# Kernel optimization log

Measured on AMD Instinct MI355X. Metric: run time of the kernel, lower is better.

## Reference

```python
import math
import jax, jax.numpy as jnp
import numpy as np

N_HEADS = 8
FACTOR = 1


def setup_inputs() -> dict:
    key = jax.random.key(0)
    ks = jax.random.split(key, 8)
    B, L, D = 8, 2048, 512
    scale = 0.05
    return {
        "queries": jax.random.normal(ks[0], (B, L, D), jnp.float32),
        "keys": jax.random.normal(ks[1], (B, L, D), jnp.float32),
        "values": jax.random.normal(ks[2], (B, L, D), jnp.float32),
        "Wq": jax.random.normal(ks[3], (D, D), jnp.float32) * scale,
        "bq": jnp.zeros((D,), jnp.float32),
        "Wk": jax.random.normal(ks[4], (D, D), jnp.float32) * scale,
        "bk": jnp.zeros((D,), jnp.float32),
        "Wv": jax.random.normal(ks[5], (D, D), jnp.float32) * scale,
        "bv": jnp.zeros((D,), jnp.float32),
        "Wo": jax.random.normal(ks[6], (D, D), jnp.float32) * scale,
        "bo": jnp.zeros((D,), jnp.float32),
    }


def _autocorrelation(q, k, v):
    # q,k,v: [B, L, H, E]; L == S assumed (as built in setup_inputs)
    B, L, H, E = q.shape
    qp = jnp.transpose(q, (0, 2, 3, 1))  # [B,H,E,L]
    kp = jnp.transpose(k, (0, 2, 3, 1))
    vp = jnp.transpose(v, (0, 2, 3, 1))
    q_fft = jnp.fft.rfft(qp, axis=-1)
    k_fft = jnp.fft.rfft(kp, axis=-1)
    corr = jnp.fft.irfft(q_fft * jnp.conj(k_fft), n=L, axis=-1)  # [B,H,E,L]

    # training-path time-delay aggregation
    top_k = int(FACTOR * math.log(L))  # static python int
    mean_value = corr.mean(axis=(1, 2))  # [B, L]
    _, index = jax.lax.top_k(mean_value.mean(axis=0), top_k)  # [K] global delays
    weights = mean_value[:, index]  # [B, K]
    tmp_corr = jax.nn.softmax(weights, axis=-1)  # [B, K]
    # roll(v, -d) along last axis == gather at (t + d) mod L
    idx = (jnp.arange(L)[None, :] + index[:, None]) % L  # [K, L]
    patterns = vp[..., idx]  # [B,H,E,K,L]
    delays_agg = jnp.einsum('bhekl,bk->bhel', patterns, tmp_corr)  # [B,H,E,L]
    return jnp.transpose(delays_agg, (0, 3, 1, 2))  # [B,L,H,E]


def reference(queries, keys, values, Wq, bq, Wk, bk, Wv, bv, Wo, bo):
    B, L, Dm = queries.shape
    H = N_HEADS
    q = (queries @ Wq + bq).reshape(B, L, H, -1)
    k = (keys @ Wk + bk).reshape(B, L, H, -1)
    v = (values @ Wv + bv).reshape(B, L, H, -1)
    out = _autocorrelation(q, k, v).reshape(B, L, -1)
    return out @ Wo + bo
```

## Files before the change

kernel.cpp:

```cpp
#include <hip/hip_runtime.h>
#include <stdint.h>

#define BATCH 8
#define L_SEQ 2048
#define D_MODEL 512
#define TOPK 7
#define BM 128
#define BN 128
#define BK 32
#define LK 40
#define LT 136

typedef _Float16 f16x8 __attribute__((ext_vector_type(8)));
typedef __attribute__((ext_vector_type(4))) float f32x4;
typedef unsigned short u16;
typedef unsigned int u32;

__device__ __forceinline__ u16 f2h(float f) {
    union { _Float16 h; u16 u; } v; v.h = (_Float16)f; return v.u;
}

__device__ __forceinline__ void load_lds16(const u16* g, u16* l) {
    __builtin_amdgcn_global_load_lds(
        (const __attribute__((address_space(1))) u32*)(g),
        (__attribute__((address_space(3))) u32*)(l), 16, 0, 0);
}

__global__ __launch_bounds__(256, 3) void gemm_qkv(
    const float* __restrict__ Xq, const float* __restrict__ Xk, const float* __restrict__ Xv,
    const u16* __restrict__ Wqt, const u16* __restrict__ Wkt, const u16* __restrict__ Wvt,
    const float* __restrict__ bq, const float* __restrict__ bk, const float* __restrict__ bv,
    u16* __restrict__ QT, u16* __restrict__ KT, u16* __restrict__ Vout)
{
    __shared__ __align__(16) u16 smem[2 * BM * LK + 2 * BN * BK];
    u16* lT = smem;
    u16* lBb = smem + 2 * BM * LK;

    const int tid = threadIdx.x;
    const int hw = blockIdx.x;
    const int lg = (hw & 7) * 192 + (hw >> 3);
    const int bn = lg & 3, bm = (lg >> 2) & 127, z = lg >> 9;

    const int lane = tid & 63, wave = tid >> 6;
    const int wm = wave >> 1, wn = wave & 1;
    const int l15 = lane & 15, quad = lane >> 4;

    const float* A  = (z == 0) ? Xq  : (z == 1) ? Xk  : Xv;
    const u16*   Bt = (z == 0) ? Wqt : (z == 1) ? Wkt : Wvt;
    const float* bias = (z == 0) ? bq : (z == 1) ? bk : bv;

    const int s0 = wave * 64 + lane, s1 = s0 + 256;
    const int r0 = s0 >> 2, c0 = (s0 & 3) ^ ((r0 >> 1) & 3);
    const int r1 = s1 >> 2, c1 = (s1 & 3) ^ ((r1 >> 1) & 3);
    const u16* gB0 = Bt + (long)(bn * BN + r0) * D_MODEL + c0 * 8;
    const u16* gB1 = Bt + (long)(bn * BN + r1) * D_MODEL + c1 * 8;

    f32x4 acc[4][4] = {};

    {
        load_lds16(gB0, lBb + wave * 512);
        load_lds16(gB1, lBb + 2048 + wave * 512);
        gB0 += BK; gB1 += BK;
        #pragma unroll
        for (int j = 0; j < 4; ++j) {
            int idx = tid + j * 256;
            int row = idx >> 3, c4 = (idx & 7) * 4;
            float4 va = *(const float4*)(A + (long)(bm * BM + row) * D_MODEL + c4);
            ushort4 pa;
            pa.x = f2h(va.x); pa.y = f2h(va.y); pa.z = f2h(va.z); pa.w = f2h(va.w);
            *(ushort4*)&smem[row * LK + c4] = pa;
        }
    }
    __syncthreads();

    for (int t = 0; t < 16; ++t) {
        const int cur = t & 1;
        u16* lAc = smem + cur * (BM * LK);
        u16* lBc = lBb + cur * (BN * BK);
        u16* lAn = smem + (cur ^ 1) * (BM * LK);
        u16* lBn = lBb + (cur ^ 1) * (BN * BK);
        const bool nx = (t < 15);
        const int k1 = (t + 1) * BK;

        float4 va[4];
        if (nx) {
            load_lds16(gB0, lBn + wave * 512);
            load_lds16(gB1, lBn + 2048 + wave * 512);
            gB0 += BK; gB1 += BK;
            #pragma unroll
            for (int j = 0; j < 4; ++j) {
                int idx = tid + j * 256;
                int row = idx >> 3, c4 = (idx & 7) * 4;
                va[j] = *(const float4*)(A + (long)(bm * BM + row) * D_MODEL + k1 + c4);
            }
        }

        f16x8 fa[4], fb[4];
        #pragma unroll
        for (int i = 0; i < 4; ++i)
            fa[i] = *(const f16x8*)&lAc[(wm * 64 + i * 16 + l15) * LK + quad * 8];
        #pragma unroll
        for (int j = 0; j < 4; ++j) {
            int n = wn * 64 + j * 16 + l15;
            int cs = quad ^ ((n >> 1) & 3);
            fb[j] = *(const f16x8*)&lBc[n * 32 + cs * 8];
        }
        #pragma unroll
        for (int i = 0; i < 4; ++i)
            #pragma unroll
            for (int j = 0; j < 4; ++j)
                acc[i][j] = __builtin_amdgcn_mfma_f32_16x16x32_f16(fa[i], fb[j], acc[i][j], 0, 0, 0);

        if (nx) {
            #pragma unroll
            for (int j = 0; j < 4; ++j) {
                int idx = tid + j * 256;
                int row = idx >> 3, c4 = (idx & 7) * 4;
                ushort4 pa;
                pa.x = f2h(va[j].x); pa.y = f2h(va[j].y);
                pa.z = f2h(va[j].z); pa.w = f2h(va[j].w);
                *(ushort4*)&lAn[row * LK + c4] = pa;
            }
        }
        __syncthreads();
    }

    if (z < 2) {
        u16* out = (z == 0) ? QT : KT;
        const int t0 = (bm * BM) & (L_SEQ - 1);
        const int bb = (bm * BM) >> 11;
        #pragma unroll
        for (int h = 0; h < 2; ++h) {
            __syncthreads();
            if (wn == h) {
                #pragma unroll
                for (int j = 0; j < 4; ++j) {
                    int dloc = j * 16 + l15;
                    float bvv = bias[bn * BN + h * 64 + dloc];
                    #pragma unroll
                    for (int i = 0; i < 4; ++i) {
                        int trow = wm * 64 + i * 16 + quad * 4;
                        #pragma unroll
                        for (int r = 0; r < 4; ++r)
                            lT[dloc * LT + trow + r] = f2h(acc[i][j][r] + bvv);
                    }
                }
            }
            __syncthreads();
            int dloc = tid >> 2, q4 = tid & 3;
            long base = ((long)(bb * D_MODEL + bn * BN + h * 64 + dloc)) * L_SEQ + t0;
            #pragma unroll
            for (int s = 0; s < 4; ++s) {
                int c = q4 * 4 + s;
                *(uint4*)(out + base + c * 8) = *(const uint4*)&lT[dloc * LT + c * 8];
            }
        }
    } else {
        #pragma unroll
        for (int i = 0; i < 4; ++i) {
            int row = bm * BM + wm * 64 + i * 16 + quad * 4;
            #pragma unroll
            for (int j = 0; j < 4; ++j) {
                int col = bn * BN + wn * 64 + j * 16 + l15;
                float bvv = bias[col];
                #pragma unroll
                for (int r = 0; r < 4; ++r)
                    Vout[(long)(row + r) * D_MODEL + col] = f2h(acc[i][j][r] + bvv);
            }
        }
    }
}

__global__ __launch_bounds__(256, 3) void gemm_out_fused(
    const u16* __restrict__ V, const u16* __restrict__ Bt,
    const int* __restrict__ selIdx, const float* __restrict__ selW,
    const float* __restrict__ bias, float* __restrict__ Cp)
{
    __shared__ __align__(16) u16 lA[2 * BM * LK];
    __shared__ __align__(16) u16 lB[2 * BN * BK];
    __shared__ int   si[TOPK];
    __shared__ float sw[BATCH][TOPK];

    const int tid = threadIdx.x;
    const int hw = blockIdx.x;
    const int lg = (hw & 7) * 64 + (hw >> 3);
    const int bn = lg & 3, bm = lg >> 2;

    const int lane = tid & 63, wave = tid >> 6;
    const int wm = wave >> 1, wn = wave & 1;
    const int l15 = lane & 15, quad = lane >> 4;

    if (tid < TOPK) si[tid] = selIdx[tid];
    if (tid < BATCH * TOPK) sw[tid / TOPK][tid % TOPK] = selW[tid];

    const int s0 = wave * 64 + lane, s1 = s0 + 256;
    const int r0 = s0 >> 2, c0 = (s0 & 3) ^ ((r0 >> 1) & 3);
    const int r1 = s1 >> 2, c1 = (s1 & 3) ^ ((r1 >> 1) & 3);
    const u16* gB0 = Bt + (long)(bn * BN + r0) * D_MODEL + c0 * 8;
    const u16* gB1 = Bt + (long)(bn * BN + r1) * D_MODEL + c1 * 8;

    const int row_a = tid >> 2,          c8_a = (tid & 3) * 8;
    const int row_b = (tid + 256) >> 2,  c8_b = (tid & 3) * 8;
    const int gra = bm * BM + row_a, grb = bm * BM + row_b;
    const int ba = gra >> 11, la = gra & (L_SEQ - 1);
    const int bb = grb >> 11, lb = grb & (L_SEQ - 1);

    __syncthreads();

    union U8 { uint4 u; _Float16 h[8]; };

    f32x4 acc[4][4] = {};

    {
        load_lds16(gB0, lB + wave * 512);
        load_lds16(gB1, lB + 2048 + wave * 512);
        gB0 += BK; gB1 += BK;
        #pragma unroll
        for (int j = 0; j < 2; ++j) {
            int row = j ? row_b : row_a, c8 = j ? c8_b : c8_a;
            int b = j ? bb : ba, l = j ? lb : la;
            float a[8] = {0,0,0,0,0,0,0,0};
            #pragma unroll
            for (int k = 0; k < TOPK; ++k) {
                int src = (l + si[k]) & (L_SEQ - 1);
                U8 x; x.u = *(const uint4*)(V + ((long)b * L_SEQ + src) * D_MODEL + c8);
                float w = sw[b][k];
                #pragma unroll
                for (int q = 0; q < 8; ++q) a[q] += w * (float)x.h[q];
            }
            union { uint4 u; u16 s[8]; } o;
            #pragma unroll
            for (int q = 0; q < 8; ++q) o.s[q] = f2h(a[q]);
            *(uint4*)&lA[row * LK + c8] = o.u;
        }
    }
    __syncthreads();

    for (int t = 0; t < 16; ++t) {
        const int cur = t & 1;
        u16* lAc = lA + cur * (BM * LK);
        u16* lBc = lB + cur * (BN * BK);
        u16* lAn = lA + (cur ^ 1) * (BM * LK);
        u16* lBn = lB + (cur ^ 1) * (BN * BK);
        const bool nx = (t < 15);
        const int k1 = (t + 1) * BK;

        U8 xv[7];
        if (nx) {
            load_lds16(gB0, lBn + wave * 512);
            load_lds16(gB1, lBn + 2048 + wave * 512);
            gB0 += BK; gB1 += BK;
            #pragma unroll
            for (int k = 0; k < TOPK; ++k) {
                int src = (la + si[k]) & (L_SEQ - 1);
                xv[k].u = *(const uint4*)(V + ((long)ba * L_SEQ + src) * D_MODEL + k1 + c8_a);
            }
        }

        f16x8 fa[4], fb[4];
        #pragma unroll
        for (int i = 0; i < 4; ++i)
            fa[i] = *(const f16x8*)&lAc[(wm * 64 + i * 16 + l15) * LK + quad * 8];
        #pragma unroll
        for (int j = 0; j < 4; ++j) {
            int n = wn * 64 + j * 16 + l15;
            int cs = quad ^ ((n >> 1) & 3);
            fb[j] = *(const f16x8*)&lBc[n * 32 + cs * 8];
        }

        #pragma unroll
        for (int i = 0; i < 2; ++i)
            #pragma unroll
            for (int j = 0; j < 4; ++j)
                acc[i][j] = __builtin_amdgcn_mfma_f32_16x16x32_f16(fa[i], fb[j], acc[i][j], 0, 0, 0);

        U8 xw[7];
        if (nx) {
            float a[8] = {0,0,0,0,0,0,0,0};
            #pragma unroll
            for (int k = 0; k < TOPK; ++k) {
                float w = sw[ba][k];
                #pragma unroll
                for (int q = 0; q < 8; ++q) a[q] += w * (float)xv[k].h[q];
            }
            union { uint4 u; u16 s[8]; } o;
            #pragma unroll
            for (int q = 0; q < 8; ++q) o.s[q] = f2h(a[q]);
            *(uint4*)&lAn[row_a * LK + c8_a] = o.u;
            #pragma unroll
            for (int k = 0; k < TOPK; ++k) {
                int src = (lb + si[k]) & (L_SEQ - 1);
                xw[k].u = *(const uint4*)(V + ((long)bb * L_SEQ + src) * D_MODEL + k1 + c8_b);
            }
        }

        #pragma unroll
        for (int i = 2; i < 4; ++i)
            #pragma unroll
            for (int j = 0; j < 4; ++j)
                acc[i][j] = __builtin_amdgcn_mfma_f32_16x16x32_f16(fa[i], fb[j], acc[i][j], 0, 0, 0);

        if (nx) {
            float a[8] = {0,0,0,0,0,0,0,0};
            #pragma unroll
            for (int k = 0; k < TOPK; ++k) {
                float w = sw[bb][k];
                #pragma unroll
                for (int q = 0; q < 8; ++q) a[q] += w * (float)xw[k].h[q];
            }
            union { uint4 u; u16 s[8]; } o;
            #pragma unroll
            for (int q = 0; q < 8; ++q) o.s[q] = f2h(a[q]);
            *(uint4*)&lAn[row_b * LK + c8_b] = o.u;
        }
        __syncthreads();
    }

    #pragma unroll
    for (int i = 0; i < 4; ++i) {
        int row = bm * BM + wm * 64 + i * 16 + quad * 4;
        #pragma unroll
        for (int j = 0; j < 4; ++j) {
            int col = bn * BN + wn * 64 + j * 16 + l15;
            float bvv = bias[col];
            #pragma unroll
            for (int r = 0; r < 4; ++r)
                Cp[(long)(row + r) * D_MODEL + col] = acc[i][j][r] + bvv;
        }
    }
}

__device__ __forceinline__ void fft2048_lds(
    float* Zr, float* Zi, const float* Twr, const float* Twi, int tid)
{
    #pragma unroll
    for (int s = 0; s < 10; s += 2) {
        #pragma unroll
        for (int u = 0; u < 2; ++u) {
            int idx = tid + u * 256;
            int d1 = 1 << s;
            int pos = idx & (d1 - 1);
            int i0 = ((idx >> s) << (s + 2)) + pos;
            float w1r = Twr[pos << (10 - s)], w1i = Twi[pos << (10 - s)];
            float w2r = Twr[pos << (9 - s)],  w2i = Twi[pos << (9 - s)];
            int p2 = pos + d1;
            float w3r = Twr[p2 << (9 - s)],   w3i = Twi[p2 << (9 - s)];
            float ar = Zr[i0],          ai = Zi[i0];
            float br = Zr[i0 + d1],     bi = Zi[i0 + d1];
            float cr = Zr[i0 + 2 * d1], ci = Zi[i0 + 2 * d1];
            float dr = Zr[i0 + 3 * d1], di = Zi[i0 + 3 * d1];
            float t1r = br * w1r - bi * w1i, t1i = br * w1i + bi * w1r;
            float Ar = ar + t1r, Ai = ai + t1i, Br = ar - t1r, Bi = ai - t1i;
            float t2r = dr * w1r - di * w1i, t2i = dr * w1i + di * w1r;
            float Cr = cr + t2r, Ci = ci + t2i, Dr = cr - t2r, Di = ci - t2i;
            float u1r = Cr * w2r - Ci * w2i, u1i = Cr * w2i + Ci * w2r;
            float u2r = Dr * w3r - Di * w3i, u2i = Dr * w3i + Di * w3r;
            Zr[i0]          = Ar + u1r; Zi[i0]          = Ai + u1i;
            Zr[i0 + 2 * d1] = Ar - u1r; Zi[i0 + 2 * d1] = Ai - u1i;
            Zr[i0 + d1]     = Br + u2r; Zi[i0 + d1]     = Bi + u2i;
            Zr[i0 + 3 * d1] = Br - u2r; Zi[i0 + 3 * d1] = Bi - u2i;
        }
        __syncthreads();
    }
    #pragma unroll
    for (int j = 0; j < 4; ++j) {
        int idx = tid + j * 256;
        float wr = Twr[idx], wi = Twi[idx];
        float ar = Zr[idx], ai = Zi[idx];
        float br = Zr[idx + 1024], bi = Zi[idx + 1024];
        float tr = br * wr - bi * wi, ti = br * wi + bi * wr;
        Zr[idx] = ar + tr; Zi[idx] = ai + ti;
        Zr[idx + 1024] = ar - tr; Zi[idx + 1024] = ai - ti;
    }
    __syncthreads();
}

__global__ __launch_bounds__(256) void fft_corr_fwd(
    const u16* __restrict__ QT, const u16* __restrict__ KT, float* __restrict__ S)
{
    __shared__ float Zr[2048], Zi[2048];
    __shared__ float Sr[2048], Si[2048];
    __shared__ float Twr[1024], Twi[1024];
    const int tid = threadIdx.x;
    const int b = blockIdx.x >> 6, dg = blockIdx.x & 63;

    #pragma unroll
    for (int j = 0; j < 4; ++j) {
        int i = tid + j * 256;
        float ang = -6.28318530717958647692f * (float)i * (1.0f / 2048.0f);
        float sn, cs; __sincosf(ang, &sn, &cs);
        Twr[i] = cs; Twi[i] = sn;
    }
    #pragma unroll
    for (int j = 0; j < 8; ++j) { Sr[tid + j * 256] = 0.f; Si[tid + j * 256] = 0.f; }

    for (int g = 0; g < 8; ++g) {
        int d = dg * 8 + g;
        const u16* qrow = QT + ((long)b * D_MODEL + d) * L_SEQ;
        const u16* krow = KT + ((long)b * D_MODEL + d) * L_SEQ;
        __syncthreads();
        union { uint4 u; _Float16 h[8]; } xq, xk;
        xq.u = *(const uint4*)(qrow + tid * 8);
        xk.u = *(const uint4*)(krow + tid * 8);
        #pragma unroll
        for (int j = 0; j < 8; ++j) {
            int t = tid * 8 + j;
            int tr = (int)(__brev((unsigned)t) >> 21);
            Zr[tr] = (float)xq.h[j];
            Zi[tr] = (float)xk.h[j];
        }
        __syncthreads();
        fft2048_lds(Zr, Zi, Twr, Twi, tid);
        #pragma unroll
        for (int j = 0; j < 8; ++j) {
            int f = tid + j * 256;
            int fm = (2048 - f) & 2047;
            float Xr = Zr[f], Xi = Zi[f], Xmr = Zr[fm], Xmi = Zi[fm];
            float qr = 0.5f * (Xr + Xmr), qi = 0.5f * (Xi - Xmi);
            float dr = Xr - Xmr,          di = Xi + Xmi;
            float kr = 0.5f * di,         ki = -0.5f * dr;
            Sr[f] += qr * kr + qi * ki;
            Si[f] += qi * kr - qr * ki;
        }
    }
    __syncthreads();
    #pragma unroll
    for (int j = 0; j < 8; ++j) {
        int f = tid + j * 256;
        atomicAdd(&S[((long)b * 2048 + f) * 2 + 0], Sr[f]);
        atomicAdd(&S[((long)b * 2048 + f) * 2 + 1], Si[f]);
    }
}

__global__ __launch_bounds__(256) void fft_corr_inv(
    const float* __restrict__ S, float* __restrict__ raw)
{
    __shared__ float Zr[2048], Zi[2048];
    __shared__ float Twr[1024], Twi[1024];
    const int tid = threadIdx.x;
    const int b = blockIdx.x;

    #pragma unroll
    for (int j = 0; j < 4; ++j) {
        int i = tid + j * 256;
        float ang = 6.28318530717958647692f * (float)i * (1.0f / 2048.0f);
        float sn, cs; __sincosf(ang, &sn, &cs);
        Twr[i] = cs; Twi[i] = sn;
    }
    #pragma unroll
    for (int j = 0; j < 8; ++j) {
        int f = tid + j * 256;
        int fr = (int)(__brev((unsigned)f) >> 21);
        Zr[fr] = S[((long)b * 2048 + f) * 2 + 0];
        Zi[fr] = S[((long)b * 2048 + f) * 2 + 1];
    }
    __syncthreads();
    fft2048_lds(Zr, Zi, Twr, Twi, tid);
    #pragma unroll
    for (int j = 0; j < 8; ++j) {
        int t = tid + j * 256;
        raw[(long)b * 2048 + t] = Zr[t] * (1.0f / 2048.0f);
    }
}

__global__ __launch_bounds__(256) void transposeW4(
    const float* __restrict__ Wq, const float* __restrict__ Wk,
    const float* __restrict__ Wv, const float* __restrict__ Wo, u16* __restrict__ dstBase)
{
    __shared__ float t[32][33];
    const int z = blockIdx.z;
    const float* src = (z == 0) ? Wq : (z == 1) ? Wk : (z == 2) ? Wv : Wo;
    u16* dst = dstBase + (long)z * D_MODEL * D_MODEL;
    int tx = threadIdx.x & 31, ty = threadIdx.x >> 5;
    int c0 = blockIdx.x * 32, r0 = blockIdx.y * 32;
    #pragma unroll
    for (int r = ty; r < 32; r += 8)
        t[r][tx] = src[(long)(r0 + r) * D_MODEL + c0 + tx];
    __syncthreads();
    #pragma unroll
    for (int r = ty; r < 32; r += 8)
        dst[(long)(c0 + r) * D_MODEL + r0 + tx] = f2h(t[tx][r]);
}

__global__ __launch_bounds__(256) void select_topk(
    const float* __restrict__ raw, int* __restrict__ selIdx, float* __restrict__ selW)
{
    __shared__ float g[L_SEQ];
    __shared__ float wv[4];
    __shared__ int   wi[4];
    __shared__ int   sidx[TOPK];
    __shared__ float wbuf[BATCH][TOPK];
    int tid = threadIdx.x;
    int lane = tid & 63, wave = tid >> 6;
    for (int t = tid; t < L_SEQ; t += 256) {
        float s = 0.0f;
        #pragma unroll
        for (int b = 0; b < BATCH; ++b) s += raw[b * L_SEQ + t];
        g[t] = s;
    }
    __syncthreads();
    for (int it = 0; it < TOPK; ++it) {
        float best = -1e30f; int bi = 0x7fffffff;
        #pragma unroll
        for (int j = 0; j < 8; ++j) {
            int t = tid + j * 256;
            float v = g[t];
            if (v > best || (v == best && t < bi)) { best = v; bi = t; }
        }
        #pragma unroll
        for (int s = 32; s > 0; s >>= 1) {
            float v2 = __shfl_xor(best, s);
            int   i2 = __shfl_xor(bi, s);
            if (v2 > best || (v2 == best && i2 < bi)) { best = v2; bi = i2; }
        }
        if (lane == 0) { wv[wave] = best; wi[wave] = bi; }
        __syncthreads();
        if (tid == 0) {
            float b0 = wv[0]; int i0 = wi[0];
            #pragma unroll
            for (int w = 1; w < 4; ++w)
                if (wv[w] > b0 || (wv[w] == b0 && wi[w] < i0)) { b0 = wv[w]; i0 = wi[w]; }
            sidx[it] = i0; g[i0] = -1e30f;
        }
        __syncthreads();
    }
    if (tid < BATCH * TOPK) {
        int b = tid / TOPK, k = tid % TOPK;
        wbuf[b][k] = raw[b * L_SEQ + sidx[k]] * (1.0f / 512.0f);
    }
    __syncthreads();
    if (tid < BATCH) {
        float mx = -1e30f;
        #pragma unroll
        for (int k = 0; k < TOPK; ++k) mx = fmaxf(mx, wbuf[tid][k]);
        float e[TOPK]; float sum = 0.0f;
        #pragma unroll
        for (int k = 0; k < TOPK; ++k) { e[k] = expf(wbuf[tid][k] - mx); sum += e[k]; }
        #pragma unroll
        for (int k = 0; k < TOPK; ++k) selW[tid * TOPK + k] = e[k] / sum;
    }
    if (tid < TOPK) selIdx[tid] = sidx[tid];
}

extern "C" void kernel_launch(void* const* d_in, const int* in_sizes, int n_in,
                              void* d_out, int out_size, void* d_ws, size_t ws_size,
                              hipStream_t stream)
{
    (void)in_sizes; (void)n_in; (void)out_size; (void)ws_size;
    const float* Xq = (const float*)d_in[0];
    const float* Xk = (const float*)d_in[1];
    const float* Xv = (const float*)d_in[2];
    const float* Wq = (const float*)d_in[3];
    const float* bq = (const float*)d_in[4];
    const float* Wk = (const float*)d_in[5];
    const float* bk = (const float*)d_in[6];
    const float* Wv = (const float*)d_in[7];
    const float* bv = (const float*)d_in[8];
    const float* Wo = (const float*)d_in[9];
    const float* bo = (const float*)d_in[10];

    char* ws = (char*)d_ws;
    const long SLABH = (long)BATCH * L_SEQ * D_MODEL * sizeof(u16);
    u16* QT   = (u16*)(ws);
    u16* KT   = (u16*)(ws + SLABH);
    u16* Vf   = (u16*)(ws + 2 * SLABH);
    const long WSZ = (long)D_MODEL * D_MODEL;
    u16* Wt   = (u16*)(ws + 3 * SLABH);
    u16* Wqt = Wt + 0 * WSZ; u16* Wkt = Wt + 1 * WSZ;
    u16* Wvt = Wt + 2 * WSZ; u16* Wot = Wt + 3 * WSZ;
    float* S   = (float*)(ws + 3 * SLABH + 4 * WSZ * sizeof(u16));
    float* raw = S + (long)BATCH * L_SEQ * 2;
    int*   sIdx = (int*)(raw + (long)BATCH * L_SEQ);
    float* sW   = (float*)(sIdx + 8);

    dim3 tb(256);
    transposeW4<<<dim3(16, 16, 4), tb, 0, stream>>>(Wq, Wk, Wv, Wo, Wt);
    hipMemsetAsync(S, 0, (long)BATCH * L_SEQ * 2 * sizeof(float), stream);

    gemm_qkv<<<dim3(1536), tb, 0, stream>>>(Xq, Xk, Xv, Wqt, Wkt, Wvt, bq, bk, bv, QT, KT, Vf);

    fft_corr_fwd<<<dim3(512), tb, 0, stream>>>(QT, KT, S);
    fft_corr_inv<<<dim3(BATCH), tb, 0, stream>>>(S, raw);
    select_topk<<<1, tb, 0, stream>>>(raw, sIdx, sW);

    gemm_out_fused<<<dim3(512), tb, 0, stream>>>(Vf, Wot, sIdx, sW, bo, (float*)d_out);
}
```

Measured before the change: 317.8 us.

## Swizzle A-tile LDS, keep spectrum accumulators in registers, raise occupancy

The A tiles in both GEMMs drop the padded LDS stride (40) for an unpadded 32-wide layout with an XOR swizzle. This cuts shared memory per block so launch bounds can rise to 4 blocks per SM. gemm_out_fused now keeps the top-k indices and weights in registers instead of LDS, which removes a barrier. fft_corr_fwd accumulates the spectrum in per-thread registers instead of LDS and doubles the grid to 1024 blocks of 4 channels each, at the cost of twice as many atomicAdds to S.

Measured after the change: 446.2 us. +40.4%, slower.

```diff
diff --git a/kernel.cpp b/kernel.cpp
--- a/kernel.cpp
+++ b/kernel.cpp
@@ -8,7 +8,6 @@
 #define BM 128
 #define BN 128
 #define BK 32
-#define LK 40
 #define LT 136
 
 typedef _Float16 f16x8 __attribute__((ext_vector_type(8)));
@@ -26,15 +25,16 @@
         (__attribute__((address_space(3))) u32*)(l), 16, 0, 0);
 }
 
-__global__ __launch_bounds__(256, 3) void gemm_qkv(
+
+__global__ __launch_bounds__(256, 4) void gemm_qkv(
     const float* __restrict__ Xq, const float* __restrict__ Xk, const float* __restrict__ Xv,
     const u16* __restrict__ Wqt, const u16* __restrict__ Wkt, const u16* __restrict__ Wvt,
     const float* __restrict__ bq, const float* __restrict__ bk, const float* __restrict__ bv,
     u16* __restrict__ QT, u16* __restrict__ KT, u16* __restrict__ Vout)
 {
-    __shared__ __align__(16) u16 smem[2 * BM * LK + 2 * BN * BK];
+    __shared__ __align__(16) u16 smem[2 * BM * 32 + 2 * BN * BK];
     u16* lT = smem;
-    u16* lBb = smem + 2 * BM * LK;
+    u16* lBb = smem + 2 * BM * 32;
 
     const int tid = threadIdx.x;
     const int hw = blockIdx.x;
@@ -65,19 +65,20 @@
         for (int j = 0; j < 4; ++j) {
             int idx = tid + j * 256;
             int row = idx >> 3, c4 = (idx & 7) * 4;
+            int cs = (((c4 >> 3) ^ (row & 3)) << 3) | (c4 & 7);
             float4 va = *(const float4*)(A + (long)(bm * BM + row) * D_MODEL + c4);
             ushort4 pa;
             pa.x = f2h(va.x); pa.y = f2h(va.y); pa.z = f2h(va.z); pa.w = f2h(va.w);
-            *(ushort4*)&smem[row * LK + c4] = pa;
+            *(ushort4*)&smem[row * 32 + cs] = pa;
         }
     }
     __syncthreads();
 
     for (int t = 0; t < 16; ++t) {
         const int cur = t & 1;
-        u16* lAc = smem + cur * (BM * LK);
+        u16* lAc = smem + cur * (BM * 32);
         u16* lBc = lBb + cur * (BN * BK);
-        u16* lAn = smem + (cur ^ 1) * (BM * LK);
+        u16* lAn = smem + (cur ^ 1) * (BM * 32);
         u16* lBn = lBb + (cur ^ 1) * (BN * BK);
         const bool nx = (t < 15);
         const int k1 = (t + 1) * BK;
@@ -97,8 +98,10 @@
 
         f16x8 fa[4], fb[4];
         #pragma unroll
-        for (int i = 0; i < 4; ++i)
-            fa[i] = *(const f16x8*)&lAc[(wm * 64 + i * 16 + l15) * LK + quad * 8];
+        for (int i = 0; i < 4; ++i) {
+            int r = wm * 64 + i * 16 + l15;
+            fa[i] = *(const f16x8*)&lAc[r * 32 + ((quad ^ (r & 3)) << 3)];
+        }
         #pragma unroll
         for (int j = 0; j < 4; ++j) {
             int n = wn * 64 + j * 16 + l15;
@@ -116,10 +119,11 @@
             for (int j = 0; j < 4; ++j) {
                 int idx = tid + j * 256;
                 int row = idx >> 3, c4 = (idx & 7) * 4;
+                int cs = (((c4 >> 3) ^ (row & 3)) << 3) | (c4 & 7);
                 ushort4 pa;
                 pa.x = f2h(va[j].x); pa.y = f2h(va[j].y);
                 pa.z = f2h(va[j].z); pa.w = f2h(va[j].w);
-                *(ushort4*)&lAn[row * LK + c4] = pa;
+                *(ushort4*)&lAn[row * 32 + cs] = pa;
             }
         }
         __syncthreads();
@@ -171,15 +175,13 @@
     }
 }
 
-__global__ __launch_bounds__(256, 3) void gemm_out_fused(
+__global__ __launch_bounds__(256, 4) void gemm_out_fused(
     const u16* __restrict__ V, const u16* __restrict__ Bt,
     const int* __restrict__ selIdx, const float* __restrict__ selW,
     const float* __restrict__ bias, float* __restrict__ Cp)
 {
-    __shared__ __align__(16) u16 lA[2 * BM * LK];
+    __shared__ __align__(16) u16 lA[2 * BM * 32];
     __shared__ __align__(16) u16 lB[2 * BN * BK];
-    __shared__ int   si[TOPK];
-    __shared__ float sw[BATCH][TOPK];
 
     const int tid = threadIdx.x;
     const int hw = blockIdx.x;
@@ -190,8 +192,9 @@
     const int wm = wave >> 1, wn = wave & 1;
     const int l15 = lane & 15, quad = lane >> 4;
 
-    if (tid < TOPK) si[tid] = selIdx[tid];
-    if (tid < BATCH * TOPK) sw[tid / TOPK][tid % TOPK] = selW[tid];
+    int   sik[TOPK];
+    #pragma unroll
+    for (int k = 0; k < TOPK; ++k) sik[k] = selIdx[k];
 
     const int s0 = wave * 64 + lane, s1 = s0 + 256;
     const int r0 = s0 >> 2, c0 = (s0 & 3) ^ ((r0 >> 1) & 3);
@@ -201,11 +204,18 @@
 
     const int row_a = tid >> 2,          c8_a = (tid & 3) * 8;
     const int row_b = (tid + 256) >> 2,  c8_b = (tid & 3) * 8;
+    const int csa = ((c8_a >> 3) ^ (row_a & 3)) << 3;
+    const int csb = ((c8_b >> 3) ^ (row_b & 3)) << 3;
     const int gra = bm * BM + row_a, grb = bm * BM + row_b;
     const int ba = gra >> 11, la = gra & (L_SEQ - 1);
     const int bb = grb >> 11, lb = grb & (L_SEQ - 1);
 
-    __syncthreads();
+    float swa[TOPK], swb[TOPK];
+    #pragma unroll
+    for (int k = 0; k < TOPK; ++k) {
+        swa[k] = selW[ba * TOPK + k];
+        swb[k] = selW[bb * TOPK + k];
+    }
 
     union U8 { uint4 u; _Float16 h[8]; };
 
@@ -215,32 +225,42 @@
         load_lds16(gB0, lB + wave * 512);
         load_lds16(gB1, lB + 2048 + wave * 512);
         gB0 += BK; gB1 += BK;
-        #pragma unroll
-        for (int j = 0; j < 2; ++j) {
-            int row = j ? row_b : row_a, c8 = j ? c8_b : c8_a;
-            int b = j ? bb : ba, l = j ? lb : la;
+        {
             float a[8] = {0,0,0,0,0,0,0,0};
             #pragma unroll
             for (int k = 0; k < TOPK; ++k) {
-                int src = (l + si[k]) & (L_SEQ - 1);
-                U8 x; x.u = *(const uint4*)(V + ((long)b * L_SEQ + src) * D_MODEL + c8);
-                float w = sw[b][k];
+                int src = (la + sik[k]) & (L_SEQ - 1);
+                U8 x; x.u = *(const uint4*)(V + ((long)ba * L_SEQ + src) * D_MODEL + c8_a);
                 #pragma unroll
-                for (int q = 0; q < 8; ++q) a[q] += w * (float)x.h[q];
+                for (int q = 0; q < 8; ++q) a[q] += swa[k] * (float)x.h[q];
             }
             union { uint4 u; u16 s[8]; } o;
             #pragma unroll
             for (int q = 0; q < 8; ++q) o.s[q] = f2h(a[q]);
-            *(uint4*)&lA[row * LK + c8] = o.u;
+            *(uint4*)&lA[row_a * 32 + csa] = o.u;
+        }
+        {
+            float a[8] = {0,0,0,0,0,0,0,0};
+            #pragma unroll
+            for (int k = 0; k < TOPK; ++k) {
+                int src = (lb + sik[k]) & (L_SEQ - 1);
+                U8 x; x.u = *(const uint4*)(V + ((long)bb * L_SEQ + src) * D_MODEL + c8_b);
+                #pragma unroll
+                for (int q = 0; q < 8; ++q) a[q] += swb[k] * (float)x.h[q];
+            }
+            union { uint4 u; u16 s[8]; } o;
+            #pragma unroll
+            for (int q = 0; q < 8; ++q) o.s[q] = f2h(a[q]);
+            *(uint4*)&lA[row_b * 32 + csb] = o.u;
         }
     }
     __syncthreads();
 
     for (int t = 0; t < 16; ++t) {
         const int cur = t & 1;
-        u16* lAc = lA + cur * (BM * LK);
+        u16* lAc = lA + cur * (BM * 32);
         u16* lBc = lB + cur * (BN * BK);
-        u16* lAn = lA + (cur ^ 1) * (BM * LK);
+        u16* lAn = lA + (cur ^ 1) * (BM * 32);
         u16* lBn = lB + (cur ^ 1) * (BN * BK);
         const bool nx = (t < 15);
         const int k1 = (t + 1) * BK;
@@ -252,15 +272,17 @@
             gB0 += BK; gB1 += BK;
             #pragma unroll
             for (int k = 0; k < TOPK; ++k) {
-                int src = (la + si[k]) & (L_SEQ - 1);
+                int src = (la + sik[k]) & (L_SEQ - 1);
                 xv[k].u = *(const uint4*)(V + ((long)ba * L_SEQ + src) * D_MODEL + k1 + c8_a);
             }
         }
 
         f16x8 fa[4], fb[4];
         #pragma unroll
-        for (int i = 0; i < 4; ++i)
-            fa[i] = *(const f16x8*)&lAc[(wm * 64 + i * 16 + l15) * LK + quad * 8];
+        for (int i = 0; i < 4; ++i) {
+            int r = wm * 64 + i * 16 + l15;
+            fa[i] = *(const f16x8*)&lAc[r * 32 + ((quad ^ (r & 3)) << 3)];
+        }
         #pragma unroll
         for (int j = 0; j < 4; ++j) {
             int n = wn * 64 + j * 16 + l15;
@@ -279,17 +301,16 @@
             float a[8] = {0,0,0,0,0,0,0,0};
             #pragma unroll
             for (int k = 0; k < TOPK; ++k) {
-                float w = sw[ba][k];
                 #pragma unroll
-                for (int q = 0; q < 8; ++q) a[q] += w * (float)xv[k].h[q];
+                for (int q = 0; q < 8; ++q) a[q] += swa[k] * (float)xv[k].h[q];
             }
             union { uint4 u; u16 s[8]; } o;
             #pragma unroll
             for (int q = 0; q < 8; ++q) o.s[q] = f2h(a[q]);
-            *(uint4*)&lAn[row_a * LK + c8_a] = o.u;
+            *(uint4*)&lAn[row_a * 32 + csa] = o.u;
             #pragma unroll
             for (int k = 0; k < TOPK; ++k) {
-                int src = (lb + si[k]) & (L_SEQ - 1);
+                int src = (lb + sik[k]) & (L_SEQ - 1);
                 xw[k].u = *(const uint4*)(V + ((long)bb * L_SEQ + src) * D_MODEL + k1 + c8_b);
             }
         }
@@ -304,14 +325,13 @@
             float a[8] = {0,0,0,0,0,0,0,0};
             #pragma unroll
             for (int k = 0; k < TOPK; ++k) {
-                float w = sw[bb][k];
                 #pragma unroll
-                for (int q = 0; q < 8; ++q) a[q] += w * (float)xw[k].h[q];
+                for (int q = 0; q < 8; ++q) a[q] += swb[k] * (float)xw[k].h[q];
             }
             union { uint4 u; u16 s[8]; } o;
             #pragma unroll
             for (int q = 0; q < 8; ++q) o.s[q] = f2h(a[q]);
-            *(uint4*)&lAn[row_b * LK + c8_b] = o.u;
+            *(uint4*)&lAn[row_b * 32 + csb] = o.u;
         }
         __syncthreads();
     }
@@ -379,10 +399,9 @@
     const u16* __restrict__ QT, const u16* __restrict__ KT, float* __restrict__ S)
 {
     __shared__ float Zr[2048], Zi[2048];
-    __shared__ float Sr[2048], Si[2048];
     __shared__ float Twr[1024], Twi[1024];
     const int tid = threadIdx.x;
-    const int b = blockIdx.x >> 6, dg = blockIdx.x & 63;
+    const int b = blockIdx.x >> 7, dg = blockIdx.x & 127;
 
     #pragma unroll
     for (int j = 0; j < 4; ++j) {
@@ -391,11 +410,12 @@
         float sn, cs; __sincosf(ang, &sn, &cs);
         Twr[i] = cs; Twi[i] = sn;
     }
-    #pragma unroll
-    for (int j = 0; j < 8; ++j) { Sr[tid + j * 256] = 0.f; Si[tid + j * 256] = 0.f; }
-
-    for (int g = 0; g < 8; ++g) {
-        int d = dg * 8 + g;
+
+    float sr[8] = {0,0,0,0,0,0,0,0};
+    float si8[8] = {0,0,0,0,0,0,0,0};
+
+    for (int g = 0; g < 4; ++g) {
+        int d = dg * 4 + g;
         const u16* qrow = QT + ((long)b * D_MODEL + d) * L_SEQ;
         const u16* krow = KT + ((long)b * D_MODEL + d) * L_SEQ;
         __syncthreads();
@@ -419,16 +439,15 @@
             float qr = 0.5f * (Xr + Xmr), qi = 0.5f * (Xi - Xmi);
             float dr = Xr - Xmr,          di = Xi + Xmi;
             float kr = 0.5f * di,         ki = -0.5f * dr;
-            Sr[f] += qr * kr + qi * ki;
-            Si[f] += qi * kr - qr * ki;
-        }
-    }
-    __syncthreads();
+            sr[j]  += qr * kr + qi * ki;
+            si8[j] += qi * kr - qr * ki;
+        }
+    }
     #pragma unroll
     for (int j = 0; j < 8; ++j) {
         int f = tid + j * 256;
-        atomicAdd(&S[((long)b * 2048 + f) * 2 + 0], Sr[f]);
-        atomicAdd(&S[((long)b * 2048 + f) * 2 + 1], Si[f]);
+        atomicAdd(&S[((long)b * 2048 + f) * 2 + 0], sr[j]);
+        atomicAdd(&S[((long)b * 2048 + f) * 2 + 1], si8[j]);
     }
 }
 
@@ -579,7 +598,7 @@
 
     gemm_qkv<<<dim3(1536), tb, 0, stream>>>(Xq, Xk, Xv, Wqt, Wkt, Wvt, bq, bk, bv, QT, KT, Vf);
 
-    fft_corr_fwd<<<dim3(512), tb, 0, stream>>>(QT, KT, S);
+    fft_corr_fwd<<<dim3(1024), tb, 0, stream>>>(QT, KT, S);
     fft_corr_inv<<<dim3(BATCH), tb, 0, stream>>>(S, raw);
     select_topk<<<1, tb, 0, stream>>>(raw, sIdx, sW);
 
```
